# Kernel optimization log

Hardware: AMD Instinct MI355X
Metric: run time of the kernel (lower is better)

Reference implementation:

```python
import jax, jax.numpy as jnp
import numpy as np

CH = 128          # channel
K = 512           # codebook_size
COMMIT_W = 1.0

def _conv(x, w, b, stride, pad):
    y = jax.lax.conv_general_dilated(
        x, w, (stride, stride), [(pad, pad), (pad, pad)],
        dimension_numbers=('NCHW', 'OIHW', 'NCHW'))
    return y + b[None, :, None, None]

def setup_inputs() -> dict:
    key = jax.random.key(0)
    ks = jax.random.split(key, 16)
    s = 0.05
    inp = {
        'x': jax.random.normal(ks[0], (64, 3, 256, 256), jnp.float32),
        # stride-2 downsampling stack: 3->32->64->128 (s_size=2, channel=128)
        'c0_w': jax.random.normal(ks[1], (32, 3, 4, 4), jnp.float32) * s,
        'c0_b': jnp.zeros((32,), jnp.float32),
        'c1_w': jax.random.normal(ks[2], (64, 32, 4, 4), jnp.float32) * s,
        'c1_b': jnp.zeros((64,), jnp.float32),
        'c2_w': jax.random.normal(ks[3], (128, 64, 4, 4), jnp.float32) * s,
        'c2_b': jnp.zeros((128,), jnp.float32),
        'c3_w': jax.random.normal(ks[4], (128, 128, 3, 3), jnp.float32) * s,
        'c3_b': jnp.zeros((128,), jnp.float32),
        # 2 ResBlocks: 128 -> 32 (3x3) -> 128 (1x1)
        'r0a_w': jax.random.normal(ks[5], (32, 128, 3, 3), jnp.float32) * s,
        'r0a_b': jnp.zeros((32,), jnp.float32),
        'r0b_w': jax.random.normal(ks[6], (128, 32, 1, 1), jnp.float32) * s,
        'r0b_b': jnp.zeros((128,), jnp.float32),
        'r1a_w': jax.random.normal(ks[7], (32, 128, 3, 3), jnp.float32) * s,
        'r1a_b': jnp.zeros((32,), jnp.float32),
        'r1b_w': jax.random.normal(ks[8], (128, 32, 1, 1), jnp.float32) * s,
        'r1b_b': jnp.zeros((128,), jnp.float32),
        'codebook': jax.random.normal(ks[9], (K, CH), jnp.float32),
    }
    return inp

def _encoder(x, c0_w, c0_b, c1_w, c1_b, c2_w, c2_b, c3_w, c3_b,
             r0a_w, r0a_b, r0b_w, r0b_b, r1a_w, r1a_b, r1b_w, r1b_b):
    x = jax.nn.relu(_conv(x, c0_w, c0_b, 2, 1))
    x = jax.nn.relu(_conv(x, c1_w, c1_b, 2, 1))
    x = jax.nn.relu(_conv(x, c2_w, c2_b, 2, 1))
    x = _conv(x, c3_w, c3_b, 1, 1)
    for ra_w, ra_b, rb_w, rb_b in ((r0a_w, r0a_b, r0b_w, r0b_b),
                                   (r1a_w, r1a_b, r1b_w, r1b_b)):
        h = jax.nn.relu(x)
        h = jax.nn.relu(_conv(h, ra_w, ra_b, 1, 1))
        h = _conv(h, rb_w, rb_b, 1, 0)
        x = x + h
    return jax.nn.relu(x)

def _vq(flat, codebook):
    # flat: (b, n, d); codebook: (K, d). Squared euclidean nearest-codeword.
    d2 = (jnp.sum(flat * flat, -1, keepdims=True)
          - 2.0 * jnp.einsum('bnd,kd->bnk', flat, codebook)
          + jnp.sum(codebook * codebook, -1))
    idx = jnp.argmin(d2, axis=-1)                 # (b, n)
    q = codebook[idx]                             # gather (b, n, d)
    commit = jnp.mean((jax.lax.stop_gradient(q) - flat) ** 2) * COMMIT_W
    q = flat + jax.lax.stop_gradient(q - flat)    # straight-through
    return q, commit

def reference(x, c0_w, c0_b, c1_w, c1_b, c2_w, c2_b, c3_w, c3_b,
              r0a_w, r0a_b, r0b_w, r0b_b, r1a_w, r1a_b, r1b_w, r1b_b,
              codebook):
    x = _encoder(x, c0_w, c0_b, c1_w, c1_b, c2_w, c2_b, c3_w, c3_b,
                 r0a_w, r0a_b, r0b_w, r0b_b, r1a_w, r1a_b, r1b_w, r1b_b)
    b, c = x.shape[0], x.shape[1]
    # faithful to torch: x.view(b, -1, c) on NCHW layout (pure reshape, no transpose)
    flat = x.reshape(b, -1, c)
    quantized, commit_loss = _vq(flat, codebook)
    return quantized, commit_loss
```

## Files before the change

kernel.cpp:

```cpp
#include <hip/hip_runtime.h>

static const size_t OFF_WT0  = 0;
static const size_t OFF_WT1  = 1536;
static const size_t OFF_WT2  = 34304;
static const size_t OFF_WT3  = 165376;
static const size_t OFF_WR0A = 312832;
static const size_t OFF_WR0B = 349696;
static const size_t OFF_WR1A = 353792;
static const size_t OFF_WR1B = 390656;
static const size_t OFF_CB2  = 394752;
static const size_t OFF_PART = 395264;
static const size_t OFF_D2   = 403456;
static const size_t OFF_IDX  = 927744;
static const size_t BASE     = 1572864;
static const size_t OFF_A0H = BASE;
static const size_t OFF_A1H = BASE + 16777216;
static const size_t OFF_A2  = BASE;
static const size_t OFF_A3  = BASE + 8388608;
static const size_t OFF_HP  = BASE + 16777216;
static const size_t OFF_A4  = BASE + 25165824;
static const size_t OFF_A5  = BASE;
static const size_t OFF_A0F = BASE;
static const size_t OFF_A1F = BASE + 33554432;
static const size_t FULL_NEED_BYTES = (BASE + 50331648) * 4;

__global__ void wtrans_kernel(const float* __restrict__ w, float* __restrict__ wt,
                              int cin, int cout, int kk) {
  int i = blockIdx.x * 256 + threadIdx.x;
  int total = cin * cout * kk;
  if (i >= total) return;
  int co = i / (cin * kk);
  int r  = i - co * cin * kk;
  wt[(size_t)r * cout + co] = w[i];
}

__global__ void cb_norm_kernel(const float* __restrict__ cb, float* __restrict__ cb2) {
  int k = blockIdx.x * 256 + threadIdx.x;
  if (k >= 512) return;
  const float4* p = (const float4*)(cb + (size_t)k * 128);
  float s = 0.f;
  for (int j = 0; j < 32; ++j) {
    float4 v = p[j];
    s += v.x * v.x; s += v.y * v.y; s += v.z * v.z; s += v.w * v.w;
  }
  cb2[k] = s;
}

template<int CIN,int COUT,int CO,int CC,int K,int S,int P,int HIN,int WIN,
         int INP,int KSPLIT,int PMODE,
         bool BIN,bool RELU_IN,bool RELU_OUT,bool ADD_RES,bool BRES>
__global__ __launch_bounds__(256, 4)
void conv_kernel(const float* __restrict__ in, const float* __restrict__ wt,
                 const float* __restrict__ bias, const float* __restrict__ res,
                 float* __restrict__ out,
                 const float* __restrict__ bias_in,
                 const float* __restrict__ bias_res)
{
  constexpr int HOUT = (HIN + 2 * P - K) / S + 1;
  constexpr int WOUT = (WIN + 2 * P - K) / S + 1;
  constexpr int TW = WOUT / 16;
  constexpr int IT = 15 * S + K;
  constexpr int NCOB = COUT / CO;
  constexpr int CINSPL = CIN / KSPLIT;
  constexpr size_t PST = (size_t)64 * CIN * HIN * WIN;
  __shared__ float in_s[CC][IT][IT + 1];

  const int tile = blockIdx.x;
  const int by   = blockIdx.y;
  const int ksl  = (KSPLIT == 1) ? 0 : (by / NCOB);
  const int co0  = ((KSPLIT == 1) ? by : (by % NCOB)) * CO;
  const int n    = blockIdx.z;
  const int th   = (tile / TW) * 16;
  const int tw   = (tile % TW) * 16;
  const int tx   = threadIdx.x & 15;
  const int ty   = threadIdx.x >> 4;

  float acc[CO];
  #pragma unroll
  for (int i = 0; i < CO; ++i) acc[i] = 0.f;

  const int ih0 = th * S - P;
  const int iw0 = tw * S - P;
  const float* inN = in + (size_t)n * CIN * HIN * WIN;

  for (int cb0 = ksl * CINSPL; cb0 < (ksl + 1) * CINSPL; cb0 += CC) {
    __syncthreads();
    for (int t = threadIdx.x; t < CC * IT * IT; t += 256) {
      int ci = t / (IT * IT);
      int rm = t - ci * IT * IT;
      int r  = rm / IT;
      int c  = rm - r * IT;
      int ih = ih0 + r, iw = iw0 + c;
      float v = 0.f;
      if (ih >= 0 && ih < HIN && iw >= 0 && iw < WIN) {
        size_t a = (size_t)(cb0 + ci) * HIN * WIN + (size_t)ih * WIN + iw;
        v = inN[a];
        if (INP >= 4) v += inN[a + PST] + inN[a + 2 * PST] + inN[a + 3 * PST];
        if (BIN) v += bias_in[cb0 + ci];
        if (RELU_IN) v = fmaxf(v, 0.f);
      }
      in_s[ci][r][c] = v;
    }
    __syncthreads();
    for (int ci = 0; ci < CC; ++ci) {
      const float* wbase = wt + ((size_t)(cb0 + ci) * K * K) * COUT + co0;
      #pragma unroll
      for (int kh = 0; kh < K; ++kh) {
        #pragma unroll
        for (int kw = 0; kw < K; ++kw) {
          float v = in_s[ci][ty * S + kh][tx * S + kw];
          const float* wrow = wbase + (size_t)(kh * K + kw) * COUT;
          #pragma unroll
          for (int co = 0; co < CO; ++co)
            acc[co] = fmaf(v, wrow[co], acc[co]);
        }
      }
    }
  }

  const int oh = th + ty, ow = tw + tx;
  const size_t HW = (size_t)HOUT * WOUT;
  const size_t pix = (size_t)oh * WOUT + ow;

  if (PMODE == 1) {
    float* outN = out + ((size_t)(ksl * 64 + n) * COUT) * HW;
    #pragma unroll
    for (int co = 0; co < CO; ++co)
      outN[(size_t)(co0 + co) * HW + pix] = acc[co];
  } else if (PMODE == 2) {
    float* outN = out + (size_t)n * COUT * HW;
    #pragma unroll
    for (int co = 0; co < CO; ++co)
      atomicAdd(&outN[(size_t)(co0 + co) * HW + pix], acc[co]);
  } else {
    float* outN = out + (size_t)n * COUT * HW;
    #pragma unroll
    for (int co = 0; co < CO; ++co) {
      float v = acc[co] + bias[co0 + co];
      if (ADD_RES) {
        float r = res[(size_t)n * COUT * HW + (size_t)(co0 + co) * HW + pix];
        if (BRES) r += bias_res[co0 + co];
        v += r;
      }
      if (RELU_OUT) v = fmaxf(v, 0.f);
      outN[(size_t)(co0 + co) * HW + pix] = v;
    }
  }
}

__global__ __launch_bounds__(256, 2)
void vq_dist_kernel(const float* __restrict__ enc, const float* __restrict__ cb,
                    const float* __restrict__ cb2, float* __restrict__ d2o,
                    int* __restrict__ io)
{
  __shared__ float cb_s[64 * 128];
  __shared__ float cb2_s[64];
  const int chunk = blockIdx.y;
  const int vec   = blockIdx.x * 256 + threadIdx.x;

  for (int t = threadIdx.x; t < 64 * 128 / 4; t += 256)
    ((float4*)cb_s)[t] = ((const float4*)(cb + (size_t)chunk * 64 * 128))[t];
  if (threadIdx.x < 64) cb2_s[threadIdx.x] = cb2[chunk * 64 + threadIdx.x];
  __syncthreads();

  float4 f[32];
  float f2 = 0.f;
  const float4* fp = (const float4*)(enc + (size_t)vec * 128);
  #pragma unroll
  for (int j = 0; j < 32; ++j) {
    float4 v = fp[j];
    v.x = fmaxf(v.x, 0.f); v.y = fmaxf(v.y, 0.f);
    v.z = fmaxf(v.z, 0.f); v.w = fmaxf(v.w, 0.f);
    f[j] = v;
    f2 += v.x * v.x; f2 += v.y * v.y; f2 += v.z * v.z; f2 += v.w * v.w;
  }

  float best = 3.0e38f;
  int bi = 0;
  for (int k = 0; k < 64; ++k) {
    const float4* ck = (const float4*)(cb_s + k * 128);
    float d0 = 0.f, d1 = 0.f, d2 = 0.f, d3 = 0.f;
    #pragma unroll
    for (int j = 0; j < 32; ++j) {
      float4 c4 = ck[j];
      d0 = fmaf(f[j].x, c4.x, d0);
      d1 = fmaf(f[j].y, c4.y, d1);
      d2 = fmaf(f[j].z, c4.z, d2);
      d3 = fmaf(f[j].w, c4.w, d3);
    }
    float dot = (d0 + d1) + (d2 + d3);
    float dist = fmaf(-2.f, dot, f2) + cb2_s[k];
    if (dist < best) { best = dist; bi = k; }
  }
  d2o[(size_t)chunk * 65536 + vec] = best;
  io [(size_t)chunk * 65536 + vec] = chunk * 64 + bi;
}

__global__ __launch_bounds__(256)
void vq_gather_kernel(const float* __restrict__ enc, const float* __restrict__ cb,
                      const float* __restrict__ d2m, const int* __restrict__ idxs,
                      float* __restrict__ out, float* __restrict__ partial)
{
  const int t   = threadIdx.x;
  const int vec = blockIdx.x * 8 + (t >> 5);
  const int j   = t & 31;

  float best = d2m[vec];
  int bi = idxs[vec];
  #pragma unroll
  for (int c = 1; c < 8; ++c) {
    float d = d2m[(size_t)c * 65536 + vec];
    int  i2 = idxs[(size_t)c * 65536 + vec];
    if (d < best) { best = d; bi = i2; }
  }

  float4 q = ((const float4*)(cb + (size_t)bi * 128))[j];
  float4 f = ((const float4*)(enc + (size_t)vec * 128))[j];
  f.x = fmaxf(f.x, 0.f); f.y = fmaxf(f.y, 0.f);
  f.z = fmaxf(f.z, 0.f); f.w = fmaxf(f.w, 0.f);
  ((float4*)out)[(size_t)vec * 32 + j] = q;

  float dx = q.x - f.x, dy = q.y - f.y, dz = q.z - f.z, dw = q.w - f.w;
  float c = dx * dx + dy * dy + dz * dz + dw * dw;
  #pragma unroll
  for (int off = 32; off > 0; off >>= 1) c += __shfl_down(c, off, 64);
  __shared__ float ls[4];
  if ((t & 63) == 0) ls[t >> 6] = c;
  __syncthreads();
  if (t == 0) partial[blockIdx.x] = (ls[0] + ls[1]) + (ls[2] + ls[3]);
}

__global__ void commit_finalize_kernel(const float* __restrict__ part,
                                       float* __restrict__ outc)
{
  __shared__ double sd[256];
  double s = 0.0;
  for (int i = threadIdx.x; i < 8192; i += 256) s += (double)part[i];
  sd[threadIdx.x] = s;
  __syncthreads();
  for (int off = 128; off > 0; off >>= 1) {
    if (threadIdx.x < off) sd[threadIdx.x] += sd[threadIdx.x + off];
    __syncthreads();
  }
  if (threadIdx.x == 0) *outc = (float)(sd[0] / 8388608.0);
}

extern "C" void kernel_launch(void* const* d_in, const int* in_sizes, int n_in,
                              void* d_out, int out_size, void* d_ws, size_t ws_size,
                              hipStream_t stream)
{
  (void)in_sizes; (void)n_in; (void)out_size;
  const float* x    = (const float*)d_in[0];
  const float* c0_w = (const float*)d_in[1];
  const float* c0_b = (const float*)d_in[2];
  const float* c1_w = (const float*)d_in[3];
  const float* c1_b = (const float*)d_in[4];
  const float* c2_w = (const float*)d_in[5];
  const float* c2_b = (const float*)d_in[6];
  const float* c3_w = (const float*)d_in[7];
  const float* c3_b = (const float*)d_in[8];
  const float* r0a_w = (const float*)d_in[9];
  const float* r0a_b = (const float*)d_in[10];
  const float* r0b_w = (const float*)d_in[11];
  const float* r0b_b = (const float*)d_in[12];
  const float* r1a_w = (const float*)d_in[13];
  const float* r1a_b = (const float*)d_in[14];
  const float* r1b_w = (const float*)d_in[15];
  const float* r1b_b = (const float*)d_in[16];
  const float* cbk   = (const float*)d_in[17];

  float* out = (float*)d_out;
  float* wsf = (float*)d_ws;

  float* WT0 = wsf + OFF_WT0;
  float* WT1 = wsf + OFF_WT1;
  float* WT2 = wsf + OFF_WT2;
  float* WT3 = wsf + OFF_WT3;
  float* WR0A = wsf + OFF_WR0A;
  float* WR0B = wsf + OFF_WR0B;
  float* WR1A = wsf + OFF_WR1A;
  float* WR1B = wsf + OFF_WR1B;
  float* CB2 = wsf + OFF_CB2;
  float* PT  = wsf + OFF_PART;
  float* D2  = wsf + OFF_D2;
  int*   IX  = (int*)(wsf + OFF_IDX);
  float* A2  = wsf + OFF_A2;
  float* A3  = wsf + OFF_A3;
  float* HP  = wsf + OFF_HP;
  float* A4  = wsf + OFF_A4;
  float* A5  = wsf + OFF_A5;

  wtrans_kernel<<<6,   256, 0, stream>>>(c0_w, WT0, 3, 32, 16);
  wtrans_kernel<<<128, 256, 0, stream>>>(c1_w, WT1, 32, 64, 16);
  wtrans_kernel<<<512, 256, 0, stream>>>(c2_w, WT2, 64, 128, 16);
  wtrans_kernel<<<576, 256, 0, stream>>>(c3_w, WT3, 128, 128, 9);
  wtrans_kernel<<<144, 256, 0, stream>>>(r0a_w, WR0A, 128, 32, 9);
  wtrans_kernel<<<16,  256, 0, stream>>>(r0b_w, WR0B, 32, 128, 1);
  wtrans_kernel<<<144, 256, 0, stream>>>(r1a_w, WR1A, 128, 32, 9);
  wtrans_kernel<<<16,  256, 0, stream>>>(r1b_w, WR1B, 32, 128, 1);
  cb_norm_kernel<<<2, 256, 0, stream>>>(cbk, CB2);

  const float* A1;
  if (ws_size >= FULL_NEED_BYTES) {
    float* A0 = wsf + OFF_A0F;
    float* A1f = wsf + OFF_A1F;
    conv_kernel<3, 32, 32, 3, 4, 2, 1, 256, 256, 1,1,0, false,false,true,false,false>
        <<<dim3(64, 1, 64), 256, 0, stream>>>(x, WT0, c0_b, nullptr, A0, nullptr, nullptr);
    conv_kernel<32, 64, 32, 8, 4, 2, 1, 128, 128, 1,1,0, false,false,true,false,false>
        <<<dim3(16, 2, 64), 256, 0, stream>>>(A0, WT1, c1_b, nullptr, A1f, nullptr, nullptr);
    A1 = A1f;
  } else {
    float* A0H = wsf + OFF_A0H;
    float* A1h = wsf + OFF_A1H;
    for (int h = 0; h < 2; ++h) {
      const float* xh = x + (size_t)h * 32 * 3 * 256 * 256;
      conv_kernel<3, 32, 32, 3, 4, 2, 1, 256, 256, 1,1,0, false,false,true,false,false>
          <<<dim3(64, 1, 32), 256, 0, stream>>>(xh, WT0, c0_b, nullptr, A0H, nullptr, nullptr);
      conv_kernel<32, 64, 32, 8, 4, 2, 1, 128, 128, 1,1,0, false,false,true,false,false>
          <<<dim3(16, 2, 32), 256, 0, stream>>>(A0H, WT1, c1_b, nullptr,
                                                A1h + (size_t)h * 32 * 64 * 64 * 64,
                                                nullptr, nullptr);
    }
    A1 = A1h;
  }

  conv_kernel<64, 128, 32, 8, 4, 2, 1, 64, 64, 1,1,0, false,false,true,false,false>
      <<<dim3(4, 4, 64), 256, 0, stream>>>(A1, WT2, c2_b, nullptr, A2, nullptr, nullptr);

  hipMemsetAsync(A3, 0, 8388608 * sizeof(float), stream);
  conv_kernel<128, 128, 32, 8, 3, 1, 1, 32, 32, 1,2,2, false,false,false,false,false>
      <<<dim3(4, 8, 64), 256, 0, stream>>>(A2, WT3, nullptr, nullptr, A3, nullptr, nullptr);

  conv_kernel<128, 32, 16, 8, 3, 1, 1, 32, 32, 1,4,1, true,true,false,false,false>
      <<<dim3(4, 8, 64), 256, 0, stream>>>(A3, WR0A, nullptr, nullptr, HP, c3_b, nullptr);
  conv_kernel<32, 128, 32, 8, 1, 1, 0, 32, 32, 4,1,0, true,true,false,true,true>
      <<<dim3(4, 4, 64), 256, 0, stream>>>(HP, WR0B, r0b_b, A3, A4, r0a_b, c3_b);
  conv_kernel<128, 32, 16, 8, 3, 1, 1, 32, 32, 1,4,1, false,true,false,false,false>
      <<<dim3(4, 8, 64), 256, 0, stream>>>(A4, WR1A, nullptr, nullptr, HP, nullptr, nullptr);
  conv_kernel<32, 128, 32, 8, 1, 1, 0, 32, 32, 4,1,0, true,true,false,true,false>
      <<<dim3(4, 4, 64), 256, 0, stream>>>(HP, WR1B, r1b_b, A4, A5, r1a_b, nullptr);

  vq_dist_kernel<<<dim3(256, 8), 256, 0, stream>>>(A5, cbk, CB2, D2, IX);
  vq_gather_kernel<<<8192, 256, 0, stream>>>(A5, cbk, D2, IX, out, PT);
  commit_finalize_kernel<<<1, 256, 0, stream>>>(PT, out + 8388608);
}
```

Baseline: 1.316 ms.

## Register-block multiple output pixels per thread in direct conv kernel

```diff
diff --git a/kernel.cpp b/kernel.cpp
--- a/kernel.cpp
+++ b/kernel.cpp
@@ -46,7 +46,7 @@
   cb2[k] = s;
 }
 
-template<int CIN,int COUT,int CO,int CC,int K,int S,int P,int HIN,int WIN,
+template<int CIN,int COUT,int CO,int CC,int K,int S,int P,int HIN,int WIN,int PX,
          int INP,int KSPLIT,int PMODE,
          bool BIN,bool RELU_IN,bool RELU_OUT,bool ADD_RES,bool BRES>
 __global__ __launch_bounds__(256, 4)
@@ -58,26 +58,30 @@
 {
   constexpr int HOUT = (HIN + 2 * P - K) / S + 1;
   constexpr int WOUT = (WIN + 2 * P - K) / S + 1;
-  constexpr int TW = WOUT / 16;
-  constexpr int IT = 15 * S + K;
+  constexpr int TWID = 16 * PX;
+  constexpr int TCOLS = WOUT / TWID;
+  constexpr int ITH = 15 * S + K;
+  constexpr int ITW = (TWID - 1) * S + K;
   constexpr int NCOB = COUT / CO;
   constexpr int CINSPL = CIN / KSPLIT;
   constexpr size_t PST = (size_t)64 * CIN * HIN * WIN;
-  __shared__ float in_s[CC][IT][IT + 1];
+  __shared__ float in_s[CC][ITH][ITW + 1];
 
   const int tile = blockIdx.x;
   const int by   = blockIdx.y;
   const int ksl  = (KSPLIT == 1) ? 0 : (by / NCOB);
   const int co0  = ((KSPLIT == 1) ? by : (by % NCOB)) * CO;
   const int n    = blockIdx.z;
-  const int th   = (tile / TW) * 16;
-  const int tw   = (tile % TW) * 16;
+  const int th   = (tile / TCOLS) * 16;
+  const int tw   = (tile % TCOLS) * TWID;
   const int tx   = threadIdx.x & 15;
   const int ty   = threadIdx.x >> 4;
 
-  float acc[CO];
-  #pragma unroll
-  for (int i = 0; i < CO; ++i) acc[i] = 0.f;
+  float acc[PX][CO];
+  #pragma unroll
+  for (int p = 0; p < PX; ++p)
+    #pragma unroll
+    for (int i = 0; i < CO; ++i) acc[p][i] = 0.f;
 
   const int ih0 = th * S - P;
   const int iw0 = tw * S - P;
@@ -85,11 +89,11 @@
 
   for (int cb0 = ksl * CINSPL; cb0 < (ksl + 1) * CINSPL; cb0 += CC) {
     __syncthreads();
-    for (int t = threadIdx.x; t < CC * IT * IT; t += 256) {
-      int ci = t / (IT * IT);
-      int rm = t - ci * IT * IT;
-      int r  = rm / IT;
-      int c  = rm - r * IT;
+    for (int t = threadIdx.x; t < CC * ITH * ITW; t += 256) {
+      int ci = t / (ITH * ITW);
+      int rm = t - ci * ITH * ITW;
+      int r  = rm / ITW;
+      int c  = rm - r * ITW;
       int ih = ih0 + r, iw = iw0 + c;
       float v = 0.f;
       if (ih >= 0 && ih < HIN && iw >= 0 && iw < WIN) {
@@ -108,42 +112,52 @@
       for (int kh = 0; kh < K; ++kh) {
         #pragma unroll
         for (int kw = 0; kw < K; ++kw) {
-          float v = in_s[ci][ty * S + kh][tx * S + kw];
           const float* wrow = wbase + (size_t)(kh * K + kw) * COUT;
+          float v[PX];
           #pragma unroll
-          for (int co = 0; co < CO; ++co)
-            acc[co] = fmaf(v, wrow[co], acc[co]);
+          for (int p = 0; p < PX; ++p)
+            v[p] = in_s[ci][ty * S + kh][(tx + 16 * p) * S + kw];
+          #pragma unroll
+          for (int co = 0; co < CO; ++co) {
+            float w = wrow[co];
+            #pragma unroll
+            for (int p = 0; p < PX; ++p)
+              acc[p][co] = fmaf(v[p], w, acc[p][co]);
+          }
         }
       }
     }
   }
 
-  const int oh = th + ty, ow = tw + tx;
+  const int oh = th + ty;
   const size_t HW = (size_t)HOUT * WOUT;
-  const size_t pix = (size_t)oh * WOUT + ow;
-
-  if (PMODE == 1) {
-    float* outN = out + ((size_t)(ksl * 64 + n) * COUT) * HW;
-    #pragma unroll
-    for (int co = 0; co < CO; ++co)
-      outN[(size_t)(co0 + co) * HW + pix] = acc[co];
-  } else if (PMODE == 2) {
-    float* outN = out + (size_t)n * COUT * HW;
-    #pragma unroll
-    for (int co = 0; co < CO; ++co)
-      atomicAdd(&outN[(size_t)(co0 + co) * HW + pix], acc[co]);
-  } else {
-    float* outN = out + (size_t)n * COUT * HW;
-    #pragma unroll
-    for (int co = 0; co < CO; ++co) {
-      float v = acc[co] + bias[co0 + co];
-      if (ADD_RES) {
-        float r = res[(size_t)n * COUT * HW + (size_t)(co0 + co) * HW + pix];
-        if (BRES) r += bias_res[co0 + co];
-        v += r;
+
+  #pragma unroll
+  for (int p = 0; p < PX; ++p) {
+    const size_t pix = (size_t)oh * WOUT + tw + tx + 16 * p;
+    if (PMODE == 1) {
+      float* outN = out + ((size_t)(ksl * 64 + n) * COUT) * HW;
+      #pragma unroll
+      for (int co = 0; co < CO; ++co)
+        outN[(size_t)(co0 + co) * HW + pix] = acc[p][co];
+    } else if (PMODE == 2) {
+      float* outN = out + (size_t)n * COUT * HW;
+      #pragma unroll
+      for (int co = 0; co < CO; ++co)
+        atomicAdd(&outN[(size_t)(co0 + co) * HW + pix], acc[p][co]);
+    } else {
+      float* outN = out + (size_t)n * COUT * HW;
+      #pragma unroll
+      for (int co = 0; co < CO; ++co) {
+        float v = acc[p][co] + bias[co0 + co];
+        if (ADD_RES) {
+          float r = res[(size_t)n * COUT * HW + (size_t)(co0 + co) * HW + pix];
+          if (BRES) r += bias_res[co0 + co];
+          v += r;
+        }
+        if (RELU_OUT) v = fmaxf(v, 0.f);
+        outN[(size_t)(co0 + co) * HW + pix] = v;
       }
-      if (RELU_OUT) v = fmaxf(v, 0.f);
-      outN[(size_t)(co0 + co) * HW + pix] = v;
     }
   }
 }
@@ -304,40 +318,40 @@
   if (ws_size >= FULL_NEED_BYTES) {
     float* A0 = wsf + OFF_A0F;
     float* A1f = wsf + OFF_A1F;
-    conv_kernel<3, 32, 32, 3, 4, 2, 1, 256, 256, 1,1,0, false,false,true,false,false>
+    conv_kernel<3, 32, 32, 3, 4, 2, 1, 256, 256, 1, 1,1,0, false,false,true,false,false>
         <<<dim3(64, 1, 64), 256, 0, stream>>>(x, WT0, c0_b, nullptr, A0, nullptr, nullptr);
-    conv_kernel<32, 64, 32, 8, 4, 2, 1, 128, 128, 1,1,0, false,false,true,false,false>
-        <<<dim3(16, 2, 64), 256, 0, stream>>>(A0, WT1, c1_b, nullptr, A1f, nullptr, nullptr);
+    conv_kernel<32, 64, 16, 4, 4, 2, 1, 128, 128, 2, 1,1,0, false,false,true,false,false>
+        <<<dim3(8, 4, 64), 256, 0, stream>>>(A0, WT1, c1_b, nullptr, A1f, nullptr, nullptr);
     A1 = A1f;
   } else {
     float* A0H = wsf + OFF_A0H;
     float* A1h = wsf + OFF_A1H;
     for (int h = 0; h < 2; ++h) {
       const float* xh = x + (size_t)h * 32 * 3 * 256 * 256;
-      conv_kernel<3, 32, 32, 3, 4, 2, 1, 256, 256, 1,1,0, false,false,true,false,false>
+      conv_kernel<3, 32, 32, 3, 4, 2, 1, 256, 256, 1, 1,1,0, false,false,true,false,false>
           <<<dim3(64, 1, 32), 256, 0, stream>>>(xh, WT0, c0_b, nullptr, A0H, nullptr, nullptr);
-      conv_kernel<32, 64, 32, 8, 4, 2, 1, 128, 128, 1,1,0, false,false,true,false,false>
-          <<<dim3(16, 2, 32), 256, 0, stream>>>(A0H, WT1, c1_b, nullptr,
-                                                A1h + (size_t)h * 32 * 64 * 64 * 64,
-                                                nullptr, nullptr);
+      conv_kernel<32, 64, 16, 4, 4, 2, 1, 128, 128, 2, 1,1,0, false,false,true,false,false>
+          <<<dim3(8, 4, 32), 256, 0, stream>>>(A0H, WT1, c1_b, nullptr,
+                                               A1h + (size_t)h * 32 * 64 * 64 * 64,
+                                               nullptr, nullptr);
     }
     A1 = A1h;
   }
 
-  conv_kernel<64, 128, 32, 8, 4, 2, 1, 64, 64, 1,1,0, false,false,true,false,false>
-      <<<dim3(4, 4, 64), 256, 0, stream>>>(A1, WT2, c2_b, nullptr, A2, nullptr, nullptr);
+  conv_kernel<64, 128, 16, 4, 4, 2, 1, 64, 64, 2, 1,1,0, false,false,true,false,false>
+      <<<dim3(2, 8, 64), 256, 0, stream>>>(A1, WT2, c2_b, nullptr, A2, nullptr, nullptr);
 
   hipMemsetAsync(A3, 0, 8388608 * sizeof(float), stream);
-  conv_kernel<128, 128, 32, 8, 3, 1, 1, 32, 32, 1,2,2, false,false,false,false,false>
-      <<<dim3(4, 8, 64), 256, 0, stream>>>(A2, WT3, nullptr, nullptr, A3, nullptr, nullptr);
-
-  conv_kernel<128, 32, 16, 8, 3, 1, 1, 32, 32, 1,4,1, true,true,false,false,false>
+  conv_kernel<128, 128, 16, 8, 3, 1, 1, 32, 32, 2, 1,2,2, false,false,false,false,false>
+      <<<dim3(2, 16, 64), 256, 0, stream>>>(A2, WT3, nullptr, nullptr, A3, nullptr, nullptr);
+
+  conv_kernel<128, 32, 16, 8, 3, 1, 1, 32, 32, 1, 1,4,1, true,true,false,false,false>
       <<<dim3(4, 8, 64), 256, 0, stream>>>(A3, WR0A, nullptr, nullptr, HP, c3_b, nullptr);
-  conv_kernel<32, 128, 32, 8, 1, 1, 0, 32, 32, 4,1,0, true,true,false,true,true>
+  conv_kernel<32, 128, 32, 8, 1, 1, 0, 32, 32, 1, 4,1,0, true,true,false,true,true>
       <<<dim3(4, 4, 64), 256, 0, stream>>>(HP, WR0B, r0b_b, A3, A4, r0a_b, c3_b);
-  conv_kernel<128, 32, 16, 8, 3, 1, 1, 32, 32, 1,4,1, false,true,false,false,false>
+  conv_kernel<128, 32, 16, 8, 3, 1, 1, 32, 32, 1, 1,4,1, false,true,false,false,false>
       <<<dim3(4, 8, 64), 256, 0, stream>>>(A4, WR1A, nullptr, nullptr, HP, nullptr, nullptr);
-  conv_kernel<32, 128, 32, 8, 1, 1, 0, 32, 32, 4,1,0, true,true,false,true,false>
+  conv_kernel<32, 128, 32, 8, 1, 1, 0, 32, 32, 1, 4,1,0, true,true,false,true,false>
       <<<dim3(4, 4, 64), 256, 0, stream>>>(HP, WR1B, r1b_b, A4, A5, r1a_b, nullptr);
 
   vq_dist_kernel<<<dim3(256, 8), 256, 0, stream>>>(A5, cbk, CB2, D2, IX);
```

After: 2.013 ms. +53.0%, slower.

## Fuse VQ distance, argmin, gather and commit loss into one kernel

Applied to the files above, without the earlier changes.

```diff
diff --git a/kernel.cpp b/kernel.cpp
--- a/kernel.cpp
+++ b/kernel.cpp
@@ -10,8 +10,6 @@
 static const size_t OFF_WR1B = 390656;
 static const size_t OFF_CB2  = 394752;
 static const size_t OFF_PART = 395264;
-static const size_t OFF_D2   = 403456;
-static const size_t OFF_IDX  = 927744;
 static const size_t BASE     = 1572864;
 static const size_t OFF_A0H = BASE;
 static const size_t OFF_A1H = BASE + 16777216;
@@ -60,6 +58,7 @@
   constexpr int WOUT = (WIN + 2 * P - K) / S + 1;
   constexpr int TW = WOUT / 16;
   constexpr int IT = 15 * S + K;
+  constexpr int KK = K * K;
   constexpr int NCOB = COUT / CO;
   constexpr int CINSPL = CIN / KSPLIT;
   constexpr size_t PST = (size_t)64 * CIN * HIN * WIN;
@@ -103,7 +102,7 @@
     }
     __syncthreads();
     for (int ci = 0; ci < CC; ++ci) {
-      const float* wbase = wt + ((size_t)(cb0 + ci) * K * K) * COUT + co0;
+      const float* wbase = wt + ((size_t)(cb0 + ci) * KK) * COUT + co0;
       #pragma unroll
       for (int kh = 0; kh < K; ++kh) {
         #pragma unroll
@@ -149,22 +148,17 @@
 }
 
 __global__ __launch_bounds__(256, 2)
-void vq_dist_kernel(const float* __restrict__ enc, const float* __restrict__ cb,
-                    const float* __restrict__ cb2, float* __restrict__ d2o,
-                    int* __restrict__ io)
+void vq_fused_kernel(const float* __restrict__ enc, const float* __restrict__ cb,
+                     const float* __restrict__ cb2, float* __restrict__ out,
+                     float* __restrict__ partial)
 {
   __shared__ float cb_s[64 * 128];
   __shared__ float cb2_s[64];
-  const int chunk = blockIdx.y;
-  const int vec   = blockIdx.x * 256 + threadIdx.x;
-
-  for (int t = threadIdx.x; t < 64 * 128 / 4; t += 256)
-    ((float4*)cb_s)[t] = ((const float4*)(cb + (size_t)chunk * 64 * 128))[t];
-  if (threadIdx.x < 64) cb2_s[threadIdx.x] = cb2[chunk * 64 + threadIdx.x];
-  __syncthreads();
+  __shared__ float red_s[256];
+  const int t   = threadIdx.x;
+  const int vec = blockIdx.x * 256 + t;
 
   float4 f[32];
-  float f2 = 0.f;
   const float4* fp = (const float4*)(enc + (size_t)vec * 128);
   #pragma unroll
   for (int j = 0; j < 32; ++j) {
@@ -172,71 +166,68 @@
     v.x = fmaxf(v.x, 0.f); v.y = fmaxf(v.y, 0.f);
     v.z = fmaxf(v.z, 0.f); v.w = fmaxf(v.w, 0.f);
     f[j] = v;
+  }
+  float f2 = 0.f;
+  #pragma unroll
+  for (int j = 0; j < 32; ++j) {
+    float4 v = f[j];
     f2 += v.x * v.x; f2 += v.y * v.y; f2 += v.z * v.z; f2 += v.w * v.w;
   }
 
   float best = 3.0e38f;
   int bi = 0;
-  for (int k = 0; k < 64; ++k) {
-    const float4* ck = (const float4*)(cb_s + k * 128);
-    float d0 = 0.f, d1 = 0.f, d2 = 0.f, d3 = 0.f;
+  for (int chunk = 0; chunk < 8; ++chunk) {
+    __syncthreads();
     #pragma unroll
-    for (int j = 0; j < 32; ++j) {
-      float4 c4 = ck[j];
-      d0 = fmaf(f[j].x, c4.x, d0);
-      d1 = fmaf(f[j].y, c4.y, d1);
-      d2 = fmaf(f[j].z, c4.z, d2);
-      d3 = fmaf(f[j].w, c4.w, d3);
-    }
-    float dot = (d0 + d1) + (d2 + d3);
-    float dist = fmaf(-2.f, dot, f2) + cb2_s[k];
-    if (dist < best) { best = dist; bi = k; }
-  }
-  d2o[(size_t)chunk * 65536 + vec] = best;
-  io [(size_t)chunk * 65536 + vec] = chunk * 64 + bi;
-}
-
-__global__ __launch_bounds__(256)
-void vq_gather_kernel(const float* __restrict__ enc, const float* __restrict__ cb,
-                      const float* __restrict__ d2m, const int* __restrict__ idxs,
-                      float* __restrict__ out, float* __restrict__ partial)
-{
-  const int t   = threadIdx.x;
-  const int vec = blockIdx.x * 8 + (t >> 5);
-  const int j   = t & 31;
-
-  float best = d2m[vec];
-  int bi = idxs[vec];
+    for (int e = 0; e < 8; ++e)
+      ((float4*)cb_s)[t + e * 256] =
+          ((const float4*)(cb + (size_t)chunk * 64 * 128))[t + e * 256];
+    if (t < 64) cb2_s[t] = cb2[chunk * 64 + t];
+    __syncthreads();
+
+    for (int k = 0; k < 64; ++k) {
+      const float4* ck = (const float4*)(cb_s + k * 128);
+      float d0 = 0.f, d1 = 0.f, d2 = 0.f, d3 = 0.f;
+      #pragma unroll
+      for (int j = 0; j < 32; ++j) {
+        float4 c4 = ck[j];
+        d0 = fmaf(f[j].x, c4.x, d0);
+        d1 = fmaf(f[j].y, c4.y, d1);
+        d2 = fmaf(f[j].z, c4.z, d2);
+        d3 = fmaf(f[j].w, c4.w, d3);
+      }
+      float dot = (d0 + d1) + (d2 + d3);
+      float dist = fmaf(-2.f, dot, f2) + cb2_s[k];
+      if (dist < best) { best = dist; bi = chunk * 64 + k; }
+    }
+  }
+
+  const float4* q4 = (const float4*)(cb + (size_t)bi * 128);
+  float4* o4 = (float4*)(out) + (size_t)vec * 32;
+  float c = 0.f;
   #pragma unroll
-  for (int c = 1; c < 8; ++c) {
-    float d = d2m[(size_t)c * 65536 + vec];
-    int  i2 = idxs[(size_t)c * 65536 + vec];
-    if (d < best) { best = d; bi = i2; }
-  }
-
-  float4 q = ((const float4*)(cb + (size_t)bi * 128))[j];
-  float4 f = ((const float4*)(enc + (size_t)vec * 128))[j];
-  f.x = fmaxf(f.x, 0.f); f.y = fmaxf(f.y, 0.f);
-  f.z = fmaxf(f.z, 0.f); f.w = fmaxf(f.w, 0.f);
-  ((float4*)out)[(size_t)vec * 32 + j] = q;
-
-  float dx = q.x - f.x, dy = q.y - f.y, dz = q.z - f.z, dw = q.w - f.w;
-  float c = dx * dx + dy * dy + dz * dz + dw * dw;
-  #pragma unroll
-  for (int off = 32; off > 0; off >>= 1) c += __shfl_down(c, off, 64);
-  __shared__ float ls[4];
-  if ((t & 63) == 0) ls[t >> 6] = c;
+  for (int j = 0; j < 32; ++j) {
+    float4 q = q4[j];
+    o4[j] = q;
+    float dx = q.x - f[j].x, dy = q.y - f[j].y;
+    float dz = q.z - f[j].z, dw = q.w - f[j].w;
+    c += dx * dx + dy * dy + dz * dz + dw * dw;
+  }
+
+  red_s[t] = c;
   __syncthreads();
-  if (t == 0) partial[blockIdx.x] = (ls[0] + ls[1]) + (ls[2] + ls[3]);
+  for (int off = 128; off > 0; off >>= 1) {
+    if (t < off) red_s[t] += red_s[t + off];
+    __syncthreads();
+  }
+  if (t == 0) partial[blockIdx.x] = red_s[0];
 }
 
 __global__ void commit_finalize_kernel(const float* __restrict__ part,
                                        float* __restrict__ outc)
 {
   __shared__ double sd[256];
-  double s = 0.0;
-  for (int i = threadIdx.x; i < 8192; i += 256) s += (double)part[i];
-  sd[threadIdx.x] = s;
+  sd[threadIdx.x] = (double)part[threadIdx.x];
   __syncthreads();
   for (int off = 128; off > 0; off >>= 1) {
     if (threadIdx.x < off) sd[threadIdx.x] += sd[threadIdx.x + off];
@@ -282,8 +273,6 @@
   float* WR1B = wsf + OFF_WR1B;
   float* CB2 = wsf + OFF_CB2;
   float* PT  = wsf + OFF_PART;
-  float* D2  = wsf + OFF_D2;
-  int*   IX  = (int*)(wsf + OFF_IDX);
   float* A2  = wsf + OFF_A2;
   float* A3  = wsf + OFF_A3;
   float* HP  = wsf + OFF_HP;
@@ -340,7 +329,6 @@
   conv_kernel<32, 128, 32, 8, 1, 1, 0, 32, 32, 4,1,0, true,true,false,true,false>
       <<<dim3(4, 4, 64), 256, 0, stream>>>(HP, WR1B, r1b_b, A4, A5, r1a_b, nullptr);
 
-  vq_dist_kernel<<<dim3(256, 8), 256, 0, stream>>>(A5, cbk, CB2, D2, IX);
-  vq_gather_kernel<<<8192, 256, 0, stream>>>(A5, cbk, D2, IX, out, PT);
+  vq_fused_kernel<<<256, 256, 0, stream>>>(A5, cbk, CB2, out, PT);
   commit_finalize_kernel<<<1, 256, 0, stream>>>(PT, out + 8388608);
 }
```

Result: slower. 1.412 ms (+7.3%).
